# Performance work log

Hardware: AMD Instinct MI355X
Metric: run time of the kernel (lower is better)

## Reference

```python
import jax, jax.numpy as jnp
import numpy as np

NX = 768
N_HEAD = 12
N_CTX = 2048
MASKED_BIAS = -10000.0


def setup_inputs() -> dict:
    key = jax.random.key(0)
    ks = jax.random.split(key, 6)
    bs, seq = 2, N_CTX
    hidden_states = jax.random.normal(ks[0], (bs, seq, NX), dtype=jnp.float32)
    attention_mask = jnp.zeros((bs, 1, 1, seq), dtype=jnp.float32)
    # Conv1D params: out = x @ W + b, W: (in, out)
    w_attn = jax.random.normal(ks[1], (NX, 3 * NX), dtype=jnp.float32) * 0.02
    b_attn = jnp.zeros((3 * NX,), dtype=jnp.float32)
    w_proj = jax.random.normal(ks[2], (NX, NX), dtype=jnp.float32) * 0.02
    b_proj = jnp.zeros((NX,), dtype=jnp.float32)
    return {
        "hidden_states": hidden_states,
        "attention_mask": attention_mask,
        "w_attn": w_attn,
        "b_attn": b_attn,
        "w_proj": w_proj,
        "b_proj": b_proj,
    }


def reference(hidden_states, attention_mask, w_attn, b_attn, w_proj, b_proj):
    bs, seq, _ = hidden_states.shape
    hd = NX // N_HEAD  # 64
    qkv = hidden_states @ w_attn + b_attn  # [bs, seq, 3*nx]
    query, key, value = jnp.split(qkv, 3, axis=2)
    # Faithful to source: direct reshape (NOT standard split-heads transpose)
    q = query.reshape(bs, N_HEAD, seq, hd)
    k = key.reshape(bs, N_HEAD, seq, hd)
    v = value.reshape(bs, N_HEAD, seq, hd)
    w = jnp.einsum("bhqd,bhkd->bhqk", q, k) / jnp.sqrt(jnp.float32(hd))
    # causal mask: tril, sliced as bias[:, :, ns-nd:ns, :ns] with nd=ns=seq
    mask = jnp.tril(jnp.ones((seq, seq), dtype=jnp.float32))[None, None]
    w = w * mask + MASKED_BIAS * (1.0 - mask)
    w = w + attention_mask
    w = jax.nn.softmax(w, axis=-1)  # dropout = identity (eval mode)
    a = jnp.einsum("bhqk,bhkd->bhqd", w, v)
    a = a.transpose(0, 2, 1, 3).reshape(bs, seq, NX)
    a = a @ w_proj + b_proj  # resid dropout = identity
    return a
```

## Files before the change

kernel.cpp:

```cpp
#include <hip/hip_runtime.h>
#include <hip/hip_bf16.h>

typedef unsigned short u16;
typedef short bf16x8 __attribute__((ext_vector_type(8)));
typedef float f32x4 __attribute__((ext_vector_type(4)));

#define NXC 768
#define NHEAD 12
#define SEQ 2048
#define BSZ 2
#define HD 64
#define NCHUNK 72
#define LOG2E 1.4426950408889634f

__device__ inline u16 f2bf(float f) {
    unsigned int u = __float_as_uint(f);
    unsigned int r = u + 0x7fffu + ((u >> 16) & 1u);
    return (u16)(r >> 16);
}
__device__ inline unsigned pk2(float lo, float hi) {
    return (unsigned)f2bf(lo) | ((unsigned)f2bf(hi) << 16);
}
__device__ inline float ex2(float x) { return __builtin_amdgcn_exp2f(x); }

__device__ inline void gld16(const u16* g, u16* l) {
    __builtin_amdgcn_global_load_lds(
        (const __attribute__((address_space(1))) unsigned int*)(g),
        (__attribute__((address_space(3))) unsigned int*)(l),
        16, 0, 0);
}

__global__ void cast4_kernel(const float* __restrict__ in, u16* __restrict__ out, int n4) {
    int i = blockIdx.x * 256 + threadIdx.x;
    if (i >= n4) return;
    float4 v = ((const float4*)in)[i];
    ushort4 o;
    o.x = f2bf(v.x); o.y = f2bf(v.y); o.z = f2bf(v.z); o.w = f2bf(v.w);
    ((ushort4*)out)[i] = o;
}

__global__ void transpose_cast_kernel(const float* __restrict__ in, u16* __restrict__ out,
                                      int R, int C) {
    __shared__ float tile[32][33];
    int cb = blockIdx.x * 32, rb = blockIdx.y * 32;
    int tx = threadIdx.x, ty = threadIdx.y;
    #pragma unroll
    for (int i = 0; i < 32; i += 8)
        tile[ty + i][tx] = in[(size_t)(rb + ty + i) * C + cb + tx];
    __syncthreads();
    #pragma unroll
    for (int i = 0; i < 32; i += 8)
        out[(size_t)(cb + ty + i) * R + rb + tx] = f2bf(tile[tx][ty + i]);
}

__global__ __launch_bounds__(256) void vt_kernel(const u16* __restrict__ Vb,
                                                 u16* __restrict__ Vtg) {
    __shared__ u16 tile[64][68];
    int y = blockIdx.y;
    size_t base = (size_t)y * (SEQ * HD);
    int ss0 = blockIdx.x * 64;
    int t = threadIdx.x;
    #pragma unroll
    for (int c = t; c < 512; c += 256) {
        int r = c >> 3, col = (c & 7) * 8;
        *(uint4*)&tile[r][col] = *(const uint4*)&Vb[base + (size_t)(ss0 + r) * HD + col];
    }
    __syncthreads();
    #pragma unroll
    for (int c = t; c < 512; c += 256) {
        int dd = c >> 3, s8 = (c & 7) * 8;
        ushort4 a, bq;
        a.x = tile[s8 + 0][dd]; a.y = tile[s8 + 1][dd];
        a.z = tile[s8 + 2][dd]; a.w = tile[s8 + 3][dd];
        bq.x = tile[s8 + 4][dd]; bq.y = tile[s8 + 5][dd];
        bq.z = tile[s8 + 6][dd]; bq.w = tile[s8 + 7][dd];
        u16* dst = &Vtg[base + (size_t)dd * SEQ + ss0 + s8];
        *(ushort4*)dst = a;
        *(ushort4*)(dst + 4) = bq;
    }
}

template <int EPI>
__global__ __launch_bounds__(256) void gemm_bt_kernel(
    const u16* __restrict__ A, const u16* __restrict__ BT,
    const float* __restrict__ bias,
    u16* __restrict__ outQ, u16* __restrict__ outK, u16* __restrict__ outV,
    float* __restrict__ outF,
    int M, int N, int K) {
    __shared__ u16 As[2 * 128 * 32];
    __shared__ u16 Bs[2 * 128 * 32];
    int tileM = blockIdx.y * 128, tileN = blockIdx.x * 128;
    int t = threadIdx.x;
    int lane = t & 63, wave = t >> 6;
    int wr = (wave >> 1) * 64, wc = (wave & 1) * 64;
    int quad = lane >> 4, l16 = lane & 15;
    f32x4 acc[4][4] = {};

    int r0 = t >> 2, c0 = (t & 3) * 8;
    const u16* Ag0 = A + (size_t)(tileM + r0) * K + c0;
    const u16* Ag1 = Ag0 + (size_t)64 * K;
    const u16* Bg0 = BT + (size_t)(tileN + r0) * K + c0;
    const u16* Bg1 = Bg0 + (size_t)64 * K;
    u16* AsW0 = As + wave * 512;
    u16* AsW1 = As + 2048 + wave * 512;
    u16* BsW0 = Bs + wave * 512;
    u16* BsW1 = Bs + 2048 + wave * 512;

    gld16(Ag0, AsW0);
    gld16(Ag1, AsW1);
    gld16(Bg0, BsW0);
    gld16(Bg1, BsW1);

    int NT = K >> 5;
    for (int tt = 0; tt < NT; ++tt) {
        int cur = tt & 1;
        if (tt + 1 < NT) {
            int kn = (tt + 1) * 32;
            int nb = (cur ^ 1) * 4096;
            gld16(Ag0 + kn, AsW0 + nb);
            gld16(Ag1 + kn, AsW1 + nb);
            gld16(Bg0 + kn, BsW0 + nb);
            gld16(Bg1 + kn, BsW1 + nb);
            asm volatile("s_waitcnt vmcnt(4)" ::: "memory");
        } else {
            asm volatile("s_waitcnt vmcnt(0)" ::: "memory");
        }
        __builtin_amdgcn_s_barrier();
        __builtin_amdgcn_sched_barrier(0);

        const u16* Ac = As + cur * 4096;
        const u16* Bc = Bs + cur * 4096;
        bf16x8 af[4], bfr[4];
        #pragma unroll
        for (int i = 0; i < 4; ++i)
            af[i] = *(const bf16x8*)&Ac[(wr + i * 16 + l16) * 32 + quad * 8];
        #pragma unroll
        for (int j = 0; j < 4; ++j)
            bfr[j] = *(const bf16x8*)&Bc[(wc + j * 16 + l16) * 32 + quad * 8];
        #pragma unroll
        for (int i = 0; i < 4; ++i)
            #pragma unroll
            for (int j = 0; j < 4; ++j)
                acc[i][j] = __builtin_amdgcn_mfma_f32_16x16x32_bf16(af[i], bfr[j], acc[i][j], 0, 0, 0);

        __builtin_amdgcn_sched_barrier(0);
        __builtin_amdgcn_s_barrier();
    }

    #pragma unroll
    for (int i = 0; i < 4; ++i) {
        #pragma unroll
        for (int j = 0; j < 4; ++j) {
            int n = tileN + wc + j * 16 + l16;
            float bv = bias[n];
            #pragma unroll
            for (int r = 0; r < 4; ++r) {
                int m = tileM + wr + i * 16 + quad * 4 + r;
                float v = acc[i][j][r] + bv;
                if (EPI == 0) {
                    if (n < 768) {
                        outQ[(size_t)m * 768 + n] = f2bf(v);
                    } else if (n < 1536) {
                        outK[(size_t)m * 768 + (n - 768)] = f2bf(v * (0.125f * LOG2E));
                    } else {
                        outV[(size_t)m * 768 + (n - 1536)] = f2bf(v);
                    }
                } else {
                    outF[(size_t)m * N + n] = v;
                }
            }
        }
    }
}

__global__ __launch_bounds__(512) void attn_mfma_kernel(
    const u16* __restrict__ Q, const u16* __restrict__ Kg,
    const u16* __restrict__ Vtg, const float* __restrict__ amask,
    u16* __restrict__ Opart, float* __restrict__ Lpart) {
    __shared__ u16 Ks[64][72];
    __shared__ u16 Vt[64][72];
    __shared__ u16 Ps[8][16][72];
    __shared__ float Ams[64];

    int bh = blockIdx.y;
    int b = bh / NHEAD, h = bh % NHEAD;
    int p = NCHUNK - 1 - (int)blockIdx.x;
    int bx = 15, c = 0, a = 0;
    #pragma unroll
    for (int i = 0; i < 16; ++i) {
        int n = (i + 2) >> 1;
        if (p < a + n) { bx = i; c = p - a; break; }
        a += n;
    }
    int kbase = c * 256;
    int nt = 2 * (bx + 1) - 4 * c;
    if (nt > 4) nt = 4;

    int t = threadIdx.x;
    int w = t >> 6, lane = t & 63;
    int quad = lane >> 4, l16 = lane & 15;
    size_t headbase = (size_t)b * (SEQ * NXC) + (size_t)h * (SEQ * HD);
    size_t headbaseT = (size_t)(b * NHEAD + h) * (SEQ * HD);

    int r0 = bx * 128;
    int qw0 = r0 + w * 16;
    int qrow = qw0 + l16;
    bf16x8 qf[2];
    #pragma unroll
    for (int s = 0; s < 2; ++s)
        qf[s] = *(const bf16x8*)&Q[headbase + (size_t)(qw0 + l16) * HD + s * 32 + quad * 8];

    float l_part = 0.f;
    f32x4 o[4] = {};

    int pr_row = t >> 3, pr_col = (t & 7) * 8;
    uint4 kr, vr; float amr;
    {
        int k0 = kbase;
        kr = *(const uint4*)&Kg[headbase + (size_t)(k0 + pr_row) * HD + pr_col];
        vr = *(const uint4*)&Vtg[headbaseT + (size_t)pr_row * SEQ + k0 + pr_col];
        if (t < 64) amr = amask[(size_t)b * SEQ + k0 + t];
    }

    for (int kt = 0; kt < nt; ++kt) {
        int k0 = kbase + kt * 64;
        __syncthreads();
        *(uint4*)&Ks[pr_row][pr_col] = kr;
        *(uint4*)&Vt[pr_row][pr_col] = vr;
        if (t < 64) Ams[t] = amr * LOG2E;
        __syncthreads();
        if (kt + 1 < nt) {
            int kn = k0 + 64;
            kr = *(const uint4*)&Kg[headbase + (size_t)(kn + pr_row) * HD + pr_col];
            vr = *(const uint4*)&Vtg[headbaseT + (size_t)pr_row * SEQ + kn + pr_col];
            if (t < 64) amr = amask[(size_t)b * SEQ + kn + t];
        }

        if (k0 > qw0 + 15) continue;

        bf16x8 kf[2][4];
        #pragma unroll
        for (int s = 0; s < 2; ++s)
            #pragma unroll
            for (int j = 0; j < 4; ++j)
                kf[s][j] = *(const bf16x8*)&Ks[j * 16 + l16][s * 32 + quad * 8];
        float amv[4][4];
        #pragma unroll
        for (int j = 0; j < 4; ++j)
            #pragma unroll
            for (int r = 0; r < 4; ++r)
                amv[j][r] = Ams[j * 16 + quad * 4 + r];

        f32x4 sacc[4] = {};
        #pragma unroll
        for (int s = 0; s < 2; ++s)
            #pragma unroll
            for (int j = 0; j < 4; ++j)
                sacc[j] = __builtin_amdgcn_mfma_f32_16x16x32_bf16(kf[s][j], qf[s], sacc[j], 0, 0, 0);

        bool diag = (k0 + 63 > qw0);
        #pragma unroll
        for (int j = 0; j < 4; ++j) {
            float pv[4];
            #pragma unroll
            for (int r = 0; r < 4; ++r) {
                float pp = ex2(sacc[j][r] + amv[j][r]);
                if (diag && (k0 + j * 16 + quad * 4 + r > qrow)) pp = 0.f;
                pv[r] = pp;
            }
            l_part += (pv[0] + pv[1]) + (pv[2] + pv[3]);
            unsigned pk01 = ((__float_as_uint(pv[0]) + 0x8000u) >> 16) |
                            ((__float_as_uint(pv[1]) + 0x8000u) & 0xffff0000u);
            unsigned pk23 = ((__float_as_uint(pv[2]) + 0x8000u) >> 16) |
                            ((__float_as_uint(pv[3]) + 0x8000u) & 0xffff0000u);
            *(uint2*)&Ps[w][l16][j * 16 + quad * 4] = make_uint2(pk01, pk23);
        }

        #pragma unroll
        for (int s = 0; s < 2; ++s) {
            bf16x8 pf = *(const bf16x8*)&Ps[w][l16][s * 32 + quad * 8];
            #pragma unroll
            for (int dc = 0; dc < 4; ++dc) {
                bf16x8 vf = *(const bf16x8*)&Vt[dc * 16 + l16][s * 32 + quad * 8];
                o[dc] = __builtin_amdgcn_mfma_f32_16x16x32_bf16(pf, vf, o[dc], 0, 0, 0);
            }
        }
    }

    float l = l_part + __shfl_xor(l_part, 16);
    l += __shfl_xor(l, 32);
    u16* Ob = Opart + ((size_t)bh * NCHUNK + p) * (128 * 64);
    float* Lb = Lpart + ((size_t)bh * NCHUNK + p) * 128;
    #pragma unroll
    for (int dc = 0; dc < 4; ++dc)
        #pragma unroll
        for (int r = 0; r < 4; ++r) {
            int rl = w * 16 + quad * 4 + r;
            Ob[rl * 64 + dc * 16 + l16] = f2bf(o[dc][r]);
        }
    if (quad == 0) Lb[w * 16 + l16] = l;
}

__global__ __launch_bounds__(256) void attn_combine_kernel(
    const u16* __restrict__ Opart, const float* __restrict__ Lpart,
    u16* __restrict__ Aout) {
    __shared__ float winv[32];
    int bh = blockIdx.y;
    int b = bh / NHEAD, h = bh % NHEAD;
    int row0 = blockIdx.x * 32;
    int bx = row0 >> 7;
    int nch = (bx + 2) >> 1;
    int m = bx >> 1;
    int p0 = (bx & 1) ? (m + 1) * (m + 1) : m * (m + 1);
    int rbase = row0 & 127;
    int t = threadIdx.x;

    if (t < 32) {
        float L = 0.f;
        for (int c = 0; c < nch; ++c)
            L += Lpart[((size_t)bh * NCHUNK + p0 + c) * 128 + rbase + t];
        winv[t] = 1.0f / L;
    }
    __syncthreads();

    int row = t >> 3;
    int d0 = (t & 7) * 8;
    int rl = rbase + row;
    float acc[8] = {};
    for (int c = 0; c < nch; ++c) {
        uint4 u = *(const uint4*)&Opart[(((size_t)bh * NCHUNK + p0 + c) * 128 + rl) * 64 + d0];
        acc[0] += __uint_as_float(u.x << 16);
        acc[1] += __uint_as_float(u.x & 0xffff0000u);
        acc[2] += __uint_as_float(u.y << 16);
        acc[3] += __uint_as_float(u.y & 0xffff0000u);
        acc[4] += __uint_as_float(u.z << 16);
        acc[5] += __uint_as_float(u.z & 0xffff0000u);
        acc[6] += __uint_as_float(u.w << 16);
        acc[7] += __uint_as_float(u.w & 0xffff0000u);
    }
    float s = winv[row];
    uint4 o;
    o.x = pk2(acc[0] * s, acc[1] * s);
    o.y = pk2(acc[2] * s, acc[3] * s);
    o.z = pk2(acc[4] * s, acc[5] * s);
    o.w = pk2(acc[6] * s, acc[7] * s);
    *(uint4*)&Aout[((size_t)b * SEQ + row0 + row) * NXC + h * HD + d0] = o;
}

extern "C" void kernel_launch(void* const* d_in, const int* in_sizes, int n_in,
                              void* d_out, int out_size, void* d_ws, size_t ws_size,
                              hipStream_t stream) {
    const float* hs     = (const float*)d_in[0];
    const float* amask  = (const float*)d_in[1];
    const float* w_attn = (const float*)d_in[2];
    const float* b_attn = (const float*)d_in[3];
    const float* w_proj = (const float*)d_in[4];
    const float* b_proj = (const float*)d_in[5];
    float* out = (float*)d_out;

    const int M = BSZ * SEQ;
    char* ws = (char*)d_ws;
    auto alloc = [&](size_t bytes) {
        char* p = ws;
        ws += (bytes + 255) & ~(size_t)255;
        return p;
    };
    u16* HSbf   = (u16*)alloc((size_t)M * NXC * 2);
    u16* WaT    = (u16*)alloc((size_t)3 * NXC * NXC * 2);
    u16* WpT    = (u16*)alloc((size_t)NXC * NXC * 2);
    u16* Qb     = (u16*)alloc((size_t)M * NXC * 2);
    u16* Kb     = (u16*)alloc((size_t)M * NXC * 2);
    u16* Vb     = (u16*)alloc((size_t)M * NXC * 2);
    u16* Vtg    = (u16*)alloc((size_t)M * NXC * 2);
    u16* Ab     = (u16*)alloc((size_t)M * NXC * 2);
    u16* Opart  = (u16*)alloc((size_t)BSZ * NHEAD * NCHUNK * 128 * 64 * 2);
    float* Lpart = (float*)alloc((size_t)BSZ * NHEAD * NCHUNK * 128 * 4);

    {
        int n4 = M * NXC / 4;
        cast4_kernel<<<dim3((n4 + 255) / 256), dim3(256), 0, stream>>>(hs, HSbf, n4);
        transpose_cast_kernel<<<dim3(3 * NXC / 32, NXC / 32), dim3(32, 8), 0, stream>>>(w_attn, WaT, NXC, 3 * NXC);
        transpose_cast_kernel<<<dim3(NXC / 32, NXC / 32), dim3(32, 8), 0, stream>>>(w_proj, WpT, NXC, NXC);
    }
    gemm_bt_kernel<0><<<dim3(3 * NXC / 128, M / 128), dim3(256), 0, stream>>>(
        HSbf, WaT, b_attn, Qb, Kb, Vb, nullptr, M, 3 * NXC, NXC);
    vt_kernel<<<dim3(SEQ / 64, BSZ * NHEAD), dim3(256), 0, stream>>>(Vb, Vtg);
    attn_mfma_kernel<<<dim3(NCHUNK, BSZ * NHEAD), dim3(512), 0, stream>>>(
        Qb, Kb, Vtg, amask, Opart, Lpart);
    attn_combine_kernel<<<dim3(SEQ / 32, BSZ * NHEAD), dim3(256), 0, stream>>>(
        Opart, Lpart, Ab);
    gemm_bt_kernel<1><<<dim3(NXC / 128, M / 128), dim3(256), 0, stream>>>(
        Ab, WpT, b_proj, nullptr, nullptr, nullptr, out, M, NXC, NXC);
}
```

Baseline: 176.3 us.

## Drop split-K attention chunks and fuse combine; merge prep casts into one kernel

Attention now gives each workgroup a full 128-row query block across the whole causal key range, with XCD-aware block ordering. It normalizes in place and writes the final bf16 output directly, so the separate combine kernel and its partial-output and partial-sum buffers are removed. The three input cast and transpose kernels are merged into one launch, and the mask values are read with a vector LDS load. This saves launches and intermediate memory traffic, but the workload per block becomes very unbalanced (2 to 32 key tiles) and the grid shrinks from 1728 to 384 workgroups, which risks a longer tail.

Measured after the change: 192.8 us. 1.09x slower.

```diff
diff --git a/kernel.cpp b/kernel.cpp
--- a/kernel.cpp
+++ b/kernel.cpp
@@ -10,7 +10,6 @@
 #define SEQ 2048
 #define BSZ 2
 #define HD 64
-#define NCHUNK 72
 #define LOG2E 1.4426950408889634f
 
 __device__ inline u16 f2bf(float f) {
@@ -30,27 +29,39 @@
         16, 0, 0);
 }
 
-__global__ void cast4_kernel(const float* __restrict__ in, u16* __restrict__ out, int n4) {
-    int i = blockIdx.x * 256 + threadIdx.x;
-    if (i >= n4) return;
-    float4 v = ((const float4*)in)[i];
-    ushort4 o;
-    o.x = f2bf(v.x); o.y = f2bf(v.y); o.z = f2bf(v.z); o.w = f2bf(v.w);
-    ((ushort4*)out)[i] = o;
-}
-
-__global__ void transpose_cast_kernel(const float* __restrict__ in, u16* __restrict__ out,
-                                      int R, int C) {
+__global__ __launch_bounds__(256) void prep_kernel(
+    const float* __restrict__ hs, u16* __restrict__ HSbf,
+    const float* __restrict__ w_attn, u16* __restrict__ WaT,
+    const float* __restrict__ w_proj, u16* __restrict__ WpT) {
     __shared__ float tile[32][33];
-    int cb = blockIdx.x * 32, rb = blockIdx.y * 32;
-    int tx = threadIdx.x, ty = threadIdx.y;
+    int blk = blockIdx.x;
+    int t = threadIdx.x;
+    if (blk < 3072) {
+        int i = blk * 256 + t;
+        float4 v = ((const float4*)hs)[i];
+        ushort4 o;
+        o.x = f2bf(v.x); o.y = f2bf(v.y); o.z = f2bf(v.z); o.w = f2bf(v.w);
+        ((ushort4*)HSbf)[i] = o;
+        return;
+    }
+    const float* in; u16* out; int C, cb, rb;
+    if (blk < 4800) {
+        int idx = blk - 3072;
+        in = w_attn; out = WaT; C = 3 * NXC;
+        cb = (idx % 72) * 32; rb = (idx / 72) * 32;
+    } else {
+        int idx = blk - 4800;
+        in = w_proj; out = WpT; C = NXC;
+        cb = (idx % 24) * 32; rb = (idx / 24) * 32;
+    }
+    int tx = t & 31, ty = t >> 5;
     #pragma unroll
     for (int i = 0; i < 32; i += 8)
         tile[ty + i][tx] = in[(size_t)(rb + ty + i) * C + cb + tx];
     __syncthreads();
     #pragma unroll
     for (int i = 0; i < 32; i += 8)
-        out[(size_t)(cb + ty + i) * R + rb + tx] = f2bf(tile[tx][ty + i]);
+        out[(size_t)(cb + ty + i) * NXC + rb + tx] = f2bf(tile[tx][ty + i]);
 }
 
 __global__ __launch_bounds__(256) void vt_kernel(const u16* __restrict__ Vb,
@@ -176,25 +187,19 @@
 __global__ __launch_bounds__(512) void attn_mfma_kernel(
     const u16* __restrict__ Q, const u16* __restrict__ Kg,
     const u16* __restrict__ Vtg, const float* __restrict__ amask,
-    u16* __restrict__ Opart, float* __restrict__ Lpart) {
+    u16* __restrict__ Aout) {
     __shared__ u16 Ks[64][72];
     __shared__ u16 Vt[64][72];
     __shared__ u16 Ps[8][16][72];
     __shared__ float Ams[64];
-
-    int bh = blockIdx.y;
+    __shared__ float Lws[8][16];
+
+    int wg = blockIdx.x;
+    int xcd = wg & 7, loc = wg >> 3;
+    int bh = xcd * 3 + (loc >> 4);
+    int bx = 15 - (loc & 15);
     int b = bh / NHEAD, h = bh % NHEAD;
-    int p = NCHUNK - 1 - (int)blockIdx.x;
-    int bx = 15, c = 0, a = 0;
-    #pragma unroll
-    for (int i = 0; i < 16; ++i) {
-        int n = (i + 2) >> 1;
-        if (p < a + n) { bx = i; c = p - a; break; }
-        a += n;
-    }
-    int kbase = c * 256;
-    int nt = 2 * (bx + 1) - 4 * c;
-    if (nt > 4) nt = 4;
+    int nt = 2 * (bx + 1);
 
     int t = threadIdx.x;
     int w = t >> 6, lane = t & 63;
@@ -216,14 +221,13 @@
     int pr_row = t >> 3, pr_col = (t & 7) * 8;
     uint4 kr, vr; float amr;
     {
-        int k0 = kbase;
-        kr = *(const uint4*)&Kg[headbase + (size_t)(k0 + pr_row) * HD + pr_col];
-        vr = *(const uint4*)&Vtg[headbaseT + (size_t)pr_row * SEQ + k0 + pr_col];
-        if (t < 64) amr = amask[(size_t)b * SEQ + k0 + t];
+        kr = *(const uint4*)&Kg[headbase + (size_t)pr_row * HD + pr_col];
+        vr = *(const uint4*)&Vtg[headbaseT + (size_t)pr_row * SEQ + pr_col];
+        if (t < 64) amr = amask[(size_t)b * SEQ + t];
     }
 
     for (int kt = 0; kt < nt; ++kt) {
-        int k0 = kbase + kt * 64;
+        int k0 = kt * 64;
         __syncthreads();
         *(uint4*)&Ks[pr_row][pr_col] = kr;
         *(uint4*)&Vt[pr_row][pr_col] = vr;
@@ -244,12 +248,10 @@
             #pragma unroll
             for (int j = 0; j < 4; ++j)
                 kf[s][j] = *(const bf16x8*)&Ks[j * 16 + l16][s * 32 + quad * 8];
-        float amv[4][4];
+        f32x4 amv4[4];
         #pragma unroll
         for (int j = 0; j < 4; ++j)
-            #pragma unroll
-            for (int r = 0; r < 4; ++r)
-                amv[j][r] = Ams[j * 16 + quad * 4 + r];
+            amv4[j] = *(const f32x4*)&Ams[j * 16 + quad * 4];
 
         f32x4 sacc[4] = {};
         #pragma unroll
@@ -264,7 +266,7 @@
             float pv[4];
             #pragma unroll
             for (int r = 0; r < 4; ++r) {
-                float pp = ex2(sacc[j][r] + amv[j][r]);
+                float pp = ex2(sacc[j][r] + amv4[j][r]);
                 if (diag && (k0 + j * 16 + quad * 4 + r > qrow)) pp = 0.f;
                 pv[r] = pp;
             }
@@ -289,62 +291,20 @@
 
     float l = l_part + __shfl_xor(l_part, 16);
     l += __shfl_xor(l, 32);
-    u16* Ob = Opart + ((size_t)bh * NCHUNK + p) * (128 * 64);
-    float* Lb = Lpart + ((size_t)bh * NCHUNK + p) * 128;
+    if (quad == 0) Lws[w][l16] = l;
+    __syncthreads();
+    float inv[4];
+    #pragma unroll
+    for (int r = 0; r < 4; ++r)
+        inv[r] = 1.0f / Lws[w][quad * 4 + r];
     #pragma unroll
     for (int dc = 0; dc < 4; ++dc)
         #pragma unroll
         for (int r = 0; r < 4; ++r) {
-            int rl = w * 16 + quad * 4 + r;
-            Ob[rl * 64 + dc * 16 + l16] = f2bf(o[dc][r]);
-        }
-    if (quad == 0) Lb[w * 16 + l16] = l;
-}
-
-__global__ __launch_bounds__(256) void attn_combine_kernel(
-    const u16* __restrict__ Opart, const float* __restrict__ Lpart,
-    u16* __restrict__ Aout) {
-    __shared__ float winv[32];
-    int bh = blockIdx.y;
-    int b = bh / NHEAD, h = bh % NHEAD;
-    int row0 = blockIdx.x * 32;
-    int bx = row0 >> 7;
-    int nch = (bx + 2) >> 1;
-    int m = bx >> 1;
-    int p0 = (bx & 1) ? (m + 1) * (m + 1) : m * (m + 1);
-    int rbase = row0 & 127;
-    int t = threadIdx.x;
-
-    if (t < 32) {
-        float L = 0.f;
-        for (int c = 0; c < nch; ++c)
-            L += Lpart[((size_t)bh * NCHUNK + p0 + c) * 128 + rbase + t];
-        winv[t] = 1.0f / L;
-    }
-    __syncthreads();
-
-    int row = t >> 3;
-    int d0 = (t & 7) * 8;
-    int rl = rbase + row;
-    float acc[8] = {};
-    for (int c = 0; c < nch; ++c) {
-        uint4 u = *(const uint4*)&Opart[(((size_t)bh * NCHUNK + p0 + c) * 128 + rl) * 64 + d0];
-        acc[0] += __uint_as_float(u.x << 16);
-        acc[1] += __uint_as_float(u.x & 0xffff0000u);
-        acc[2] += __uint_as_float(u.y << 16);
-        acc[3] += __uint_as_float(u.y & 0xffff0000u);
-        acc[4] += __uint_as_float(u.z << 16);
-        acc[5] += __uint_as_float(u.z & 0xffff0000u);
-        acc[6] += __uint_as_float(u.w << 16);
-        acc[7] += __uint_as_float(u.w & 0xffff0000u);
-    }
-    float s = winv[row];
-    uint4 o;
-    o.x = pk2(acc[0] * s, acc[1] * s);
-    o.y = pk2(acc[2] * s, acc[3] * s);
-    o.z = pk2(acc[4] * s, acc[5] * s);
-    o.w = pk2(acc[6] * s, acc[7] * s);
-    *(uint4*)&Aout[((size_t)b * SEQ + row0 + row) * NXC + h * HD + d0] = o;
+            int srow = r0 + w * 16 + quad * 4 + r;
+            Aout[((size_t)b * SEQ + srow) * NXC + h * HD + dc * 16 + l16] =
+                f2bf(o[dc][r] * inv[r]);
+        }
 }
 
 extern "C" void kernel_launch(void* const* d_in, const int* in_sizes, int n_in,
@@ -373,22 +333,13 @@
     u16* Vb     = (u16*)alloc((size_t)M * NXC * 2);
     u16* Vtg    = (u16*)alloc((size_t)M * NXC * 2);
     u16* Ab     = (u16*)alloc((size_t)M * NXC * 2);
-    u16* Opart  = (u16*)alloc((size_t)BSZ * NHEAD * NCHUNK * 128 * 64 * 2);
-    float* Lpart = (float*)alloc((size_t)BSZ * NHEAD * NCHUNK * 128 * 4);
-
-    {
-        int n4 = M * NXC / 4;
-        cast4_kernel<<<dim3((n4 + 255) / 256), dim3(256), 0, stream>>>(hs, HSbf, n4);
-        transpose_cast_kernel<<<dim3(3 * NXC / 32, NXC / 32), dim3(32, 8), 0, stream>>>(w_attn, WaT, NXC, 3 * NXC);
-        transpose_cast_kernel<<<dim3(NXC / 32, NXC / 32), dim3(32, 8), 0, stream>>>(w_proj, WpT, NXC, NXC);
-    }
+
+    prep_kernel<<<dim3(5376), dim3(256), 0, stream>>>(hs, HSbf, w_attn, WaT, w_proj, WpT);
     gemm_bt_kernel<0><<<dim3(3 * NXC / 128, M / 128), dim3(256), 0, stream>>>(
         HSbf, WaT, b_attn, Qb, Kb, Vb, nullptr, M, 3 * NXC, NXC);
     vt_kernel<<<dim3(SEQ / 64, BSZ * NHEAD), dim3(256), 0, stream>>>(Vb, Vtg);
-    attn_mfma_kernel<<<dim3(NCHUNK, BSZ * NHEAD), dim3(512), 0, stream>>>(
-        Qb, Kb, Vtg, amask, Opart, Lpart);
-    attn_combine_kernel<<<dim3(SEQ / 32, BSZ * NHEAD), dim3(256), 0, stream>>>(
-        Opart, Lpart, Ab);
+    attn_mfma_kernel<<<dim3(384), dim3(512), 0, stream>>>(
+        Qb, Kb, Vtg, amask, Ab);
     gemm_bt_kernel<1><<<dim3(NXC / 128, M / 128), dim3(256), 0, stream>>>(
         Ab, WpT, b_proj, nullptr, nullptr, nullptr, out, M, NXC, NXC);
 }
```

## Merge prep casts into one kernel and read K/V fragments directly from global

Applied to the files above, without the earlier changes.

The three fp32-to-bf16 cast and transpose launches are merged into a single prep kernel, which saves two launches. The attention kernel drops its shared-memory staging of K, V^T and the mask, along with the two block barriers per tile. Each wave now loads its MFMA fragments straight from global memory and stops early with break instead of continue. This removes the barriers and the LDS traffic, but the eight waves of a block each fetch the same K/V data, so more load traffic falls on L1/L2 and software prefetch is lost. The P buffer padding also changes.

Result: slower. 260.6 us (+47.8%).

```diff
diff --git a/kernel.cpp b/kernel.cpp
--- a/kernel.cpp
+++ b/kernel.cpp
@@ -30,27 +30,39 @@
         16, 0, 0);
 }
 
-__global__ void cast4_kernel(const float* __restrict__ in, u16* __restrict__ out, int n4) {
-    int i = blockIdx.x * 256 + threadIdx.x;
-    if (i >= n4) return;
-    float4 v = ((const float4*)in)[i];
-    ushort4 o;
-    o.x = f2bf(v.x); o.y = f2bf(v.y); o.z = f2bf(v.z); o.w = f2bf(v.w);
-    ((ushort4*)out)[i] = o;
-}
-
-__global__ void transpose_cast_kernel(const float* __restrict__ in, u16* __restrict__ out,
-                                      int R, int C) {
+__global__ __launch_bounds__(256) void prep_kernel(
+    const float* __restrict__ hs, u16* __restrict__ HSbf,
+    const float* __restrict__ w_attn, u16* __restrict__ WaT,
+    const float* __restrict__ w_proj, u16* __restrict__ WpT) {
     __shared__ float tile[32][33];
-    int cb = blockIdx.x * 32, rb = blockIdx.y * 32;
-    int tx = threadIdx.x, ty = threadIdx.y;
+    int blk = blockIdx.x;
+    int t = threadIdx.x;
+    if (blk < 3072) {
+        int i = blk * 256 + t;
+        float4 v = ((const float4*)hs)[i];
+        ushort4 o;
+        o.x = f2bf(v.x); o.y = f2bf(v.y); o.z = f2bf(v.z); o.w = f2bf(v.w);
+        ((ushort4*)HSbf)[i] = o;
+        return;
+    }
+    const float* in; u16* out; int C, cb, rb;
+    if (blk < 4800) {
+        int idx = blk - 3072;
+        in = w_attn; out = WaT; C = 3 * NXC;
+        cb = (idx % 72) * 32; rb = (idx / 72) * 32;
+    } else {
+        int idx = blk - 4800;
+        in = w_proj; out = WpT; C = NXC;
+        cb = (idx % 24) * 32; rb = (idx / 24) * 32;
+    }
+    int tx = t & 31, ty = t >> 5;
     #pragma unroll
     for (int i = 0; i < 32; i += 8)
         tile[ty + i][tx] = in[(size_t)(rb + ty + i) * C + cb + tx];
     __syncthreads();
     #pragma unroll
     for (int i = 0; i < 32; i += 8)
-        out[(size_t)(cb + ty + i) * R + rb + tx] = f2bf(tile[tx][ty + i]);
+        out[(size_t)(cb + ty + i) * NXC + rb + tx] = f2bf(tile[tx][ty + i]);
 }
 
 __global__ __launch_bounds__(256) void vt_kernel(const u16* __restrict__ Vb,
@@ -177,10 +189,7 @@
     const u16* __restrict__ Q, const u16* __restrict__ Kg,
     const u16* __restrict__ Vtg, const float* __restrict__ amask,
     u16* __restrict__ Opart, float* __restrict__ Lpart) {
-    __shared__ u16 Ks[64][72];
-    __shared__ u16 Vt[64][72];
-    __shared__ u16 Ps[8][16][72];
-    __shared__ float Ams[64];
+    __shared__ u16 Ps[8][16][76];
 
     int bh = blockIdx.y;
     int b = bh / NHEAD, h = bh % NHEAD;
@@ -202,8 +211,7 @@
     size_t headbase = (size_t)b * (SEQ * NXC) + (size_t)h * (SEQ * HD);
     size_t headbaseT = (size_t)(b * NHEAD + h) * (SEQ * HD);
 
-    int r0 = bx * 128;
-    int qw0 = r0 + w * 16;
+    int qw0 = bx * 128 + w * 16;
     int qrow = qw0 + l16;
     bf16x8 qf[2];
     #pragma unroll
@@ -213,43 +221,21 @@
     float l_part = 0.f;
     f32x4 o[4] = {};
 
-    int pr_row = t >> 3, pr_col = (t & 7) * 8;
-    uint4 kr, vr; float amr;
-    {
-        int k0 = kbase;
-        kr = *(const uint4*)&Kg[headbase + (size_t)(k0 + pr_row) * HD + pr_col];
-        vr = *(const uint4*)&Vtg[headbaseT + (size_t)pr_row * SEQ + k0 + pr_col];
-        if (t < 64) amr = amask[(size_t)b * SEQ + k0 + t];
-    }
-
     for (int kt = 0; kt < nt; ++kt) {
         int k0 = kbase + kt * 64;
-        __syncthreads();
-        *(uint4*)&Ks[pr_row][pr_col] = kr;
-        *(uint4*)&Vt[pr_row][pr_col] = vr;
-        if (t < 64) Ams[t] = amr * LOG2E;
-        __syncthreads();
-        if (kt + 1 < nt) {
-            int kn = k0 + 64;
-            kr = *(const uint4*)&Kg[headbase + (size_t)(kn + pr_row) * HD + pr_col];
-            vr = *(const uint4*)&Vtg[headbaseT + (size_t)pr_row * SEQ + kn + pr_col];
-            if (t < 64) amr = amask[(size_t)b * SEQ + kn + t];
-        }
-
-        if (k0 > qw0 + 15) continue;
+        if (k0 > qw0 + 15) break;
 
         bf16x8 kf[2][4];
         #pragma unroll
         for (int s = 0; s < 2; ++s)
             #pragma unroll
             for (int j = 0; j < 4; ++j)
-                kf[s][j] = *(const bf16x8*)&Ks[j * 16 + l16][s * 32 + quad * 8];
-        float amv[4][4];
+                kf[s][j] = *(const bf16x8*)&Kg[headbase +
+                    (size_t)(k0 + j * 16 + l16) * HD + s * 32 + quad * 8];
+        f32x4 amv4[4];
         #pragma unroll
         for (int j = 0; j < 4; ++j)
-            #pragma unroll
-            for (int r = 0; r < 4; ++r)
-                amv[j][r] = Ams[j * 16 + quad * 4 + r];
+            amv4[j] = *(const f32x4*)&amask[(size_t)b * SEQ + k0 + j * 16 + quad * 4];
 
         f32x4 sacc[4] = {};
         #pragma unroll
@@ -264,7 +250,7 @@
             float pv[4];
             #pragma unroll
             for (int r = 0; r < 4; ++r) {
-                float pp = ex2(sacc[j][r] + amv[j][r]);
+                float pp = ex2(sacc[j][r] + amv4[j][r] * LOG2E);
                 if (diag && (k0 + j * 16 + quad * 4 + r > qrow)) pp = 0.f;
                 pv[r] = pp;
             }
@@ -281,7 +267,8 @@
             bf16x8 pf = *(const bf16x8*)&Ps[w][l16][s * 32 + quad * 8];
             #pragma unroll
             for (int dc = 0; dc < 4; ++dc) {
-                bf16x8 vf = *(const bf16x8*)&Vt[dc * 16 + l16][s * 32 + quad * 8];
+                bf16x8 vf = *(const bf16x8*)&Vtg[headbaseT +
+                    (size_t)(dc * 16 + l16) * SEQ + k0 + s * 32 + quad * 8];
                 o[dc] = __builtin_amdgcn_mfma_f32_16x16x32_bf16(pf, vf, o[dc], 0, 0, 0);
             }
         }
@@ -376,12 +363,7 @@
     u16* Opart  = (u16*)alloc((size_t)BSZ * NHEAD * NCHUNK * 128 * 64 * 2);
     float* Lpart = (float*)alloc((size_t)BSZ * NHEAD * NCHUNK * 128 * 4);
 
-    {
-        int n4 = M * NXC / 4;
-        cast4_kernel<<<dim3((n4 + 255) / 256), dim3(256), 0, stream>>>(hs, HSbf, n4);
-        transpose_cast_kernel<<<dim3(3 * NXC / 32, NXC / 32), dim3(32, 8), 0, stream>>>(w_attn, WaT, NXC, 3 * NXC);
-        transpose_cast_kernel<<<dim3(NXC / 32, NXC / 32), dim3(32, 8), 0, stream>>>(w_proj, WpT, NXC, NXC);
-    }
+    prep_kernel<<<dim3(5376), dim3(256), 0, stream>>>(hs, HSbf, w_attn, WaT, w_proj, WpT);
     gemm_bt_kernel<0><<<dim3(3 * NXC / 128, M / 128), dim3(256), 0, stream>>>(
         HSbf, WaT, b_attn, Qb, Kb, Vb, nullptr, M, 3 * NXC, NXC);
     vt_kernel<<<dim3(SEQ / 64, BSZ * NHEAD), dim3(256), 0, stream>>>(Vb, Vtg);
```
